# Kernel optimization log

Measured on AMD Instinct MI355X. Metric: run time of the kernel, lower is better.

Reference implementation:

```python
import jax, jax.numpy as jnp
import numpy as np

N_NODES = 100000
N_EDGES = 1600000
IN_F, HID, EMB = 128, 64, 32


def setup_inputs() -> dict:
    key = jax.random.key(0)
    ks = jax.random.split(key, 10)
    x = jax.random.normal(ks[0], (N_NODES, IN_F), dtype=jnp.float32)
    edge_index = jax.random.randint(ks[1], (2, N_EDGES), 0, N_NODES, dtype=jnp.int64)
    s = lambda k, sh, fan_in: jax.random.normal(k, sh, dtype=jnp.float32) / jnp.sqrt(jnp.float32(fan_in))
    return {
        "x": x,
        "edge_index": edge_index,
        # SAGEConv1: lin_l (applied to aggregated neighbors, with bias) + lin_r (root, no bias)
        "W1_l": s(ks[2], (IN_F, HID), IN_F), "b1": jnp.zeros((HID,), jnp.float32), "W1_r": s(ks[3], (IN_F, HID), IN_F),
        # SAGEConv2
        "W2_l": s(ks[4], (HID, EMB), HID), "b2": jnp.zeros((EMB,), jnp.float32), "W2_r": s(ks[5], (HID, EMB), HID),
        # risk head
        "Wh": s(ks[6], (EMB, 1), EMB), "bh": jnp.zeros((1,), jnp.float32),
    }


def _sage_conv(x, src, dst, W_l, b, W_r):
    # gather messages from source nodes, segment-mean at destination nodes
    msg_sum = jax.ops.segment_sum(x[src], dst, num_segments=N_NODES)  # [N, F]
    cnt = jax.ops.segment_sum(jnp.ones((src.shape[0],), x.dtype), dst, num_segments=N_NODES)
    mean_agg = msg_sum / jnp.maximum(cnt, 1.0)[:, None]  # isolated nodes -> 0
    return mean_agg @ W_l + b + x @ W_r


def reference(x, edge_index, W1_l, b1, W1_r, W2_l, b2, W2_r, Wh, bh):
    src, dst = edge_index[0], edge_index[1]
    h = jax.nn.relu(_sage_conv(x, src, dst, W1_l, b1, W1_r))
    # dropout is identity in eval mode
    embeddings = jax.nn.relu(_sage_conv(h, src, dst, W2_l, b2, W2_r))
    risk_scores = embeddings @ Wh + bh
    return embeddings, risk_scores
```

## Files before the change

### kernel.cpp

```cpp
#include <hip/hip_runtime.h>
#include <hip/hip_bf16.h>

#define N_NODES 100000
#define N_EDGES 1600000
#define NBUCK   196
#define BSHIFT  9
#define BCAP    12288

typedef __bf16 bf16x8 __attribute__((ext_vector_type(8)));
typedef float  f32x4  __attribute__((ext_vector_type(4)));
typedef float  f32x2  __attribute__((ext_vector_type(2)));


__device__ inline unsigned char enc_fp8(float v) {
    return (unsigned char)(__builtin_amdgcn_cvt_pk_fp8_f32(v, v, 0, 0) & 0xFF);
}

__global__ __launch_bounds__(256) void partition_k(const int* __restrict__ ei,
                                                   int* __restrict__ gcur,
                                                   unsigned* __restrict__ bbuf) {
    __shared__ int hist[NBUCK];
    __shared__ int cur[NBUCK];
    int t = threadIdx.x;
    for (int i = t; i < NBUCK; i += 256) hist[i] = 0;
    __syncthreads();
    int base = blockIdx.x * 4096;
    unsigned pk[16];
    int bk[16];
#pragma unroll
    for (int i = 0; i < 16; ++i) {
        int e = base + t + i * 256;
        if (e < N_EDGES) {
            int s = ei[e], d = ei[N_EDGES + e];
            int b = d >> BSHIFT;
            pk[i] = ((unsigned)(d & 511) << 17) | (unsigned)s;
            bk[i] = b;
            atomicAdd(&hist[b], 1);
        } else bk[i] = -1;
    }
    __syncthreads();
    for (int i = t; i < NBUCK; i += 256)
        cur[i] = atomicAdd(&gcur[i], hist[i]);
    __syncthreads();
#pragma unroll
    for (int i = 0; i < 16; ++i) {
        if (bk[i] >= 0) {
            int pos = atomicAdd(&cur[bk[i]], 1);
            bbuf[(size_t)bk[i] * BCAP + pos] = pk[i];
        }
    }
}

__global__ __launch_bounds__(256) void bucketcsr_k(const unsigned* __restrict__ bbuf,
                                                   const int* __restrict__ gcur,
                                                   int* __restrict__ cnt,
                                                   int* __restrict__ offsets,
                                                   int* __restrict__ csr) {
    __shared__ int lcnt[512];
    __shared__ int loff[512];
    __shared__ int lcur[512];
    __shared__ int ssum[256];
    int b = blockIdx.x, t = threadIdx.x;
    int m = gcur[b];
    const unsigned* src = bbuf + (size_t)b * BCAP;
    for (int i = t; i < 512; i += 256) lcnt[i] = 0;
    __syncthreads();
    for (int i = t; i < m; i += 256) atomicAdd(&lcnt[src[i] >> 17], 1);
    __syncthreads();
    int a0 = lcnt[2 * t], a1 = lcnt[2 * t + 1];
    int p0 = (a0 + 3) & ~3, p1 = (a1 + 3) & ~3;
    ssum[t] = p0 + p1;
    __syncthreads();
    for (int off = 1; off < 256; off <<= 1) {
        int v = (t >= off) ? ssum[t - off] : 0;
        __syncthreads();
        ssum[t] += v;
        __syncthreads();
    }
    int ebase = (t == 0) ? 0 : ssum[t - 1];
    loff[2 * t] = ebase;
    loff[2 * t + 1] = ebase + p0;
    __syncthreads();
    for (int i = t; i < 512; i += 256) lcur[i] = loff[i];
    int nbase = b << BSHIFT;
    for (int i = t; i < 512; i += 256) {
        int n = nbase + i;
        if (n < N_NODES) {
            cnt[n] = lcnt[i];
            offsets[n] = b * BCAP + loff[i];
        }
    }
    __syncthreads();
    for (int i = t; i < m; i += 256) {
        unsigned p = src[i];
        int pos = atomicAdd(&lcur[p >> 17], 1);
        csr[(size_t)b * BCAP + pos] = (int)(p & 0x1FFFF);
    }
}

__global__ __launch_bounds__(256) void gemm1_k(const float* __restrict__ x,
                                               const float* __restrict__ W1l,
                                               const float* __restrict__ W1r,
                                               unsigned char* __restrict__ c1l,
                                               __bf16* __restrict__ c1r) {
    __shared__ __bf16 Bt[128 * 136];
    int tid = threadIdx.x;
    for (int idx = tid; idx < 8192; idx += 256) {
        int k = idx >> 6, n = idx & 63;
        Bt[n * 136 + k]        = (__bf16)W1l[idx];
        Bt[(n + 64) * 136 + k] = (__bf16)W1r[idx];
    }
    __syncthreads();

    int lane = tid & 63, wave = tid >> 6;
    int mbase = blockIdx.x * 64 + wave * 16;
    int col  = lane & 15;
    int kgrp = (lane >> 4) << 3;
    int mrow = mbase + col;
    int mclamp = mrow < N_NODES ? mrow : N_NODES - 1;
    const float* arow = x + (size_t)mclamp * 128;

    f32x4 acc[8];
#pragma unroll
    for (int i = 0; i < 8; ++i) acc[i] = (f32x4){0.f, 0.f, 0.f, 0.f};

#pragma unroll
    for (int ks = 0; ks < 4; ++ks) {
        int kk = ks * 32 + kgrp;
        f32x4 a0 = *(const f32x4*)(arow + kk);
        f32x4 a1 = *(const f32x4*)(arow + kk + 4);
        bf16x8 a;
#pragma unroll
        for (int i = 0; i < 4; ++i) { a[i] = (__bf16)a0[i]; a[i + 4] = (__bf16)a1[i]; }
#pragma unroll
        for (int nt = 0; nt < 8; ++nt) {
            bf16x8 b = *(const bf16x8*)(Bt + (nt * 16 + col) * 136 + kk);
            acc[nt] = __builtin_amdgcn_mfma_f32_16x16x32_bf16(a, b, acc[nt], 0, 0, 0);
        }
    }

    int r0 = mbase + ((lane >> 4) << 2);
#pragma unroll
    for (int r = 0; r < 4; ++r) {
        int m = r0 + r;
        if (m < N_NODES) {
#pragma unroll
            for (int nt = 0; nt < 4; ++nt)
                c1l[(size_t)m * 64 + nt * 16 + col] = enc_fp8(acc[nt][r]);
#pragma unroll
            for (int nt = 4; nt < 8; ++nt)
                c1r[(size_t)m * 64 + (nt - 4) * 16 + col] = (__bf16)acc[nt][r];
        }
    }
}

__global__ __launch_bounds__(256) void agg1_k(const unsigned char* __restrict__ c1l,
                                              const __bf16* __restrict__ c1r,
                                              const int* __restrict__ offsets,
                                              const int* __restrict__ cnt,
                                              const int* __restrict__ csr,
                                              const float* __restrict__ b1,
                                              __bf16* __restrict__ h) {
    int wave = blockIdx.x * 4 + (threadIdx.x >> 6);
    int lane = threadIdx.x & 63;
    int g = lane >> 3;
    int n = wave * 8 + g;
    int f8b = (lane & 7) << 3;
    int beg = offsets[n], deg = cnt[n];
    int end = beg + deg;
    bf16x8 rv = *(const bf16x8*)(c1r + (size_t)n * 64 + f8b);
    const int4* csr4 = (const int4*)csr;
    float sum[8];
#pragma unroll
    for (int j = 0; j < 8; ++j) sum[j] = 0.f;
    for (int e = beg; e < end; e += 8) {
        int4 i0 = csr4[e >> 2];
        int4 i1 = csr4[(e >> 2) + 1];
        int sidx[8] = {i0.x, i0.y, i0.z, i0.w, i1.x, i1.y, i1.z, i1.w};
        uint2 w[8];
#pragma unroll
        for (int u = 0; u < 8; ++u) {
            w[u].x = 0u; w[u].y = 0u;
            if (e + u < end)
                w[u] = *(const uint2*)(c1l + (size_t)sidx[u] * 64 + f8b);
        }
#pragma unroll
        for (int u = 0; u < 8; ++u) {
            f32x2 p0 = __builtin_amdgcn_cvt_pk_f32_fp8(w[u].x, 0);
            f32x2 p1 = __builtin_amdgcn_cvt_pk_f32_fp8(w[u].x, 1);
            f32x2 p2 = __builtin_amdgcn_cvt_pk_f32_fp8(w[u].y, 0);
            f32x2 p3 = __builtin_amdgcn_cvt_pk_f32_fp8(w[u].y, 1);
            sum[0] += p0[0]; sum[1] += p0[1];
            sum[2] += p1[0]; sum[3] += p1[1];
            sum[4] += p2[0]; sum[5] += p2[1];
            sum[6] += p3[0]; sum[7] += p3[1];
        }
    }
    float cf = deg > 0 ? (float)deg : 1.f;
    bf16x8 o;
#pragma unroll
    for (int j = 0; j < 8; ++j) {
        float v = sum[j] / cf + (float)rv[j] + b1[f8b + j];
        o[j] = (__bf16)(v > 0.f ? v : 0.f);
    }
    *(bf16x8*)(h + (size_t)n * 64 + f8b) = o;
}

__global__ __launch_bounds__(256) void gemm2_k(const __bf16* __restrict__ h,
                                               const float* __restrict__ W2l,
                                               const float* __restrict__ W2r,
                                               unsigned char* __restrict__ c2l,
                                               float* __restrict__ c2r) {
    __shared__ __bf16 Bt[64 * 72];
    int tid = threadIdx.x;
    for (int idx = tid; idx < 2048; idx += 256) {
        int k = idx >> 5, n = idx & 31;
        Bt[n * 72 + k]        = (__bf16)W2l[idx];
        Bt[(n + 32) * 72 + k] = (__bf16)W2r[idx];
    }
    __syncthreads();

    int lane = tid & 63, wave = tid >> 6;
    int mbase = blockIdx.x * 64 + wave * 16;
    int col  = lane & 15;
    int kgrp = (lane >> 4) << 3;
    int mrow = mbase + col;
    int mclamp = mrow < N_NODES ? mrow : N_NODES - 1;
    const __bf16* arow = h + (size_t)mclamp * 64;

    f32x4 acc[4];
#pragma unroll
    for (int i = 0; i < 4; ++i) acc[i] = (f32x4){0.f, 0.f, 0.f, 0.f};

#pragma unroll
    for (int ks = 0; ks < 2; ++ks) {
        int kk = ks * 32 + kgrp;
        bf16x8 a = *(const bf16x8*)(arow + kk);
#pragma unroll
        for (int nt = 0; nt < 4; ++nt) {
            bf16x8 b = *(const bf16x8*)(Bt + (nt * 16 + col) * 72 + kk);
            acc[nt] = __builtin_amdgcn_mfma_f32_16x16x32_bf16(a, b, acc[nt], 0, 0, 0);
        }
    }

    int r0 = mbase + ((lane >> 4) << 2);
#pragma unroll
    for (int r = 0; r < 4; ++r) {
        int m = r0 + r;
        if (m < N_NODES) {
#pragma unroll
            for (int nt = 0; nt < 2; ++nt)
                c2l[(size_t)m * 32 + nt * 16 + col] = enc_fp8(acc[nt][r]);
#pragma unroll
            for (int nt = 2; nt < 4; ++nt)
                c2r[(size_t)m * 32 + (nt - 2) * 16 + col] = acc[nt][r];
        }
    }
}

__global__ __launch_bounds__(256) void agg2_k(const unsigned char* __restrict__ c2l,
                                              const float* __restrict__ c2r,
                                              const int* __restrict__ offsets,
                                              const int* __restrict__ cnt,
                                              const int* __restrict__ csr,
                                              const float* __restrict__ b2,
                                              const float* __restrict__ Wh,
                                              const float* __restrict__ bh,
                                              float* __restrict__ out) {
    int wave = blockIdx.x * 4 + (threadIdx.x >> 6);
    int lane = threadIdx.x & 63;
    int g = lane >> 2;
    int n = wave * 16 + g;
    int f8b = (lane & 3) << 3;
    bool valid = n < N_NODES;
    int nc = valid ? n : N_NODES - 1;
    int beg = offsets[nc], deg = valid ? cnt[n] : 0;
    int end = beg + deg;
    f32x4 rr0 = *(const f32x4*)(c2r + (size_t)nc * 32 + f8b);
    f32x4 rr1 = *(const f32x4*)(c2r + (size_t)nc * 32 + f8b + 4);
    f32x4 wh0 = *(const f32x4*)(Wh + f8b);
    f32x4 wh1 = *(const f32x4*)(Wh + f8b + 4);
    const int4* csr4 = (const int4*)csr;
    float sum[8];
#pragma unroll
    for (int j = 0; j < 8; ++j) sum[j] = 0.f;
    for (int e = beg; e < end; e += 8) {
        int4 i0 = csr4[e >> 2];
        int4 i1 = csr4[(e >> 2) + 1];
        int sidx[8] = {i0.x, i0.y, i0.z, i0.w, i1.x, i1.y, i1.z, i1.w};
        uint2 w[8];
#pragma unroll
        for (int u = 0; u < 8; ++u) {
            w[u].x = 0u; w[u].y = 0u;
            if (e + u < end)
                w[u] = *(const uint2*)(c2l + (size_t)sidx[u] * 32 + f8b);
        }
#pragma unroll
        for (int u = 0; u < 8; ++u) {
            f32x2 p0 = __builtin_amdgcn_cvt_pk_f32_fp8(w[u].x, 0);
            f32x2 p1 = __builtin_amdgcn_cvt_pk_f32_fp8(w[u].x, 1);
            f32x2 p2 = __builtin_amdgcn_cvt_pk_f32_fp8(w[u].y, 0);
            f32x2 p3 = __builtin_amdgcn_cvt_pk_f32_fp8(w[u].y, 1);
            sum[0] += p0[0]; sum[1] += p0[1];
            sum[2] += p1[0]; sum[3] += p1[1];
            sum[4] += p2[0]; sum[5] += p2[1];
            sum[6] += p3[0]; sum[7] += p3[1];
        }
    }
    float cf = deg > 0 ? (float)deg : 1.f;
    float r = 0.f;
    f32x4 o0, o1;
#pragma unroll
    for (int j = 0; j < 8; ++j) {
        float root = (j < 4) ? rr0[j] : rr1[j - 4];
        float whj  = (j < 4) ? wh0[j] : wh1[j - 4];
        float v = sum[j] / cf + root + b2[f8b + j];
        v = v > 0.f ? v : 0.f;
        if (j < 4) o0[j] = v; else o1[j - 4] = v;
        r += v * whj;
    }
    if (valid) {
        *(f32x4*)(out + (size_t)n * 32 + f8b) = o0;
        *(f32x4*)(out + (size_t)n * 32 + f8b + 4) = o1;
    }
    r += __shfl_xor(r, 1, 64);
    r += __shfl_xor(r, 2, 64);
    if (valid && (lane & 3) == 0)
        out[(size_t)N_NODES * 32 + n] = r + bh[0];
}

extern "C" void kernel_launch(void* const* d_in, const int* in_sizes, int n_in,
                              void* d_out, int out_size, void* d_ws, size_t ws_size,
                              hipStream_t stream) {
    const float* x   = (const float*)d_in[0];
    const int*   ei  = (const int*)d_in[1];
    const float* W1l = (const float*)d_in[2];
    const float* b1  = (const float*)d_in[3];
    const float* W1r = (const float*)d_in[4];
    const float* W2l = (const float*)d_in[5];
    const float* b2  = (const float*)d_in[6];
    const float* W2r = (const float*)d_in[7];
    const float* Wh  = (const float*)d_in[8];
    const float* bh  = (const float*)d_in[9];
    float* out = (float*)d_out;

    char* ws = (char*)d_ws;
    unsigned char* c1l = (unsigned char*)(ws);
    __bf16*   c1r     = (__bf16*)(ws + 6400000);
    __bf16*   h       = (__bf16*)(ws + 19200000);
    unsigned char* c2l = (unsigned char*)(ws + 32000000);
    float*    c2r     = (float*)(ws + 35200000);
    int*      cnt     = (int*)(ws + 48000000);
    int*      offsets = (int*)(ws + 48400000);
    int*      gcur    = (int*)(ws + 48800000);
    unsigned* bbuf    = (unsigned*)(ws + 48804096);
    int*      csr     = (int*)(ws + 58437888);

    hipMemsetAsync(gcur, 0, NBUCK * 4, stream);

    partition_k<<<391, 256, 0, stream>>>(ei, gcur, bbuf);
    bucketcsr_k<<<NBUCK, 256, 0, stream>>>(bbuf, gcur, cnt, offsets, csr);
    gemm1_k    <<<1563, 256, 0, stream>>>(x, W1l, W1r, c1l, c1r);
    agg1_k     <<<3125, 256, 0, stream>>>(c1l, c1r, offsets, cnt, csr, b1, h);
    gemm2_k    <<<1563, 256, 0, stream>>>(h, W2l, W2r, c2l, c2r);
    agg2_k     <<<1563, 256, 0, stream>>>(c2l, c2r, offsets, cnt, csr, b2, Wh, bh, out);
}
```

Before: 221.0 us.

## Merge CSR build with gemm1 and fuse layer-1 aggregation into gemm2

The bucket-to-CSR pass and the first GEMM are independent, so they now run as one launch: the first NBUCK blocks build the CSR and the remaining blocks do the x·W1 GEMM. The layer-1 mean aggregation is fused into the second GEMM, with each block aggregating 64 nodes into a shared-memory tile of h and running the MFMA on it directly. This removes two launches and the global write and re-read of h. In exchange the fused kernel holds more LDS per block, which may lower occupancy, and each wave now aggregates two node groups serially.

```diff
diff --git a/kernel.cpp b/kernel.cpp
--- a/kernel.cpp
+++ b/kernel.cpp
@@ -51,182 +51,190 @@
     }
 }
 
-__global__ __launch_bounds__(256) void bucketcsr_k(const unsigned* __restrict__ bbuf,
+__global__ __launch_bounds__(256) void csr_gemm1_k(const unsigned* __restrict__ bbuf,
                                                    const int* __restrict__ gcur,
                                                    int* __restrict__ cnt,
                                                    int* __restrict__ offsets,
-                                                   int* __restrict__ csr) {
-    __shared__ int lcnt[512];
-    __shared__ int loff[512];
-    __shared__ int lcur[512];
-    __shared__ int ssum[256];
-    int b = blockIdx.x, t = threadIdx.x;
-    int m = gcur[b];
-    const unsigned* src = bbuf + (size_t)b * BCAP;
-    for (int i = t; i < 512; i += 256) lcnt[i] = 0;
-    __syncthreads();
-    for (int i = t; i < m; i += 256) atomicAdd(&lcnt[src[i] >> 17], 1);
-    __syncthreads();
-    int a0 = lcnt[2 * t], a1 = lcnt[2 * t + 1];
-    int p0 = (a0 + 3) & ~3, p1 = (a1 + 3) & ~3;
-    ssum[t] = p0 + p1;
-    __syncthreads();
-    for (int off = 1; off < 256; off <<= 1) {
-        int v = (t >= off) ? ssum[t - off] : 0;
-        __syncthreads();
-        ssum[t] += v;
-        __syncthreads();
-    }
-    int ebase = (t == 0) ? 0 : ssum[t - 1];
-    loff[2 * t] = ebase;
-    loff[2 * t + 1] = ebase + p0;
-    __syncthreads();
-    for (int i = t; i < 512; i += 256) lcur[i] = loff[i];
-    int nbase = b << BSHIFT;
-    for (int i = t; i < 512; i += 256) {
-        int n = nbase + i;
-        if (n < N_NODES) {
-            cnt[n] = lcnt[i];
-            offsets[n] = b * BCAP + loff[i];
-        }
-    }
-    __syncthreads();
-    for (int i = t; i < m; i += 256) {
-        unsigned p = src[i];
-        int pos = atomicAdd(&lcur[p >> 17], 1);
-        csr[(size_t)b * BCAP + pos] = (int)(p & 0x1FFFF);
-    }
-}
-
-__global__ __launch_bounds__(256) void gemm1_k(const float* __restrict__ x,
-                                               const float* __restrict__ W1l,
-                                               const float* __restrict__ W1r,
-                                               unsigned char* __restrict__ c1l,
-                                               __bf16* __restrict__ c1r) {
-    __shared__ __bf16 Bt[128 * 136];
-    int tid = threadIdx.x;
-    for (int idx = tid; idx < 8192; idx += 256) {
-        int k = idx >> 6, n = idx & 63;
-        Bt[n * 136 + k]        = (__bf16)W1l[idx];
-        Bt[(n + 64) * 136 + k] = (__bf16)W1r[idx];
-    }
-    __syncthreads();
-
-    int lane = tid & 63, wave = tid >> 6;
-    int mbase = blockIdx.x * 64 + wave * 16;
-    int col  = lane & 15;
-    int kgrp = (lane >> 4) << 3;
-    int mrow = mbase + col;
-    int mclamp = mrow < N_NODES ? mrow : N_NODES - 1;
-    const float* arow = x + (size_t)mclamp * 128;
-
-    f32x4 acc[8];
-#pragma unroll
-    for (int i = 0; i < 8; ++i) acc[i] = (f32x4){0.f, 0.f, 0.f, 0.f};
-
-#pragma unroll
-    for (int ks = 0; ks < 4; ++ks) {
-        int kk = ks * 32 + kgrp;
-        f32x4 a0 = *(const f32x4*)(arow + kk);
-        f32x4 a1 = *(const f32x4*)(arow + kk + 4);
-        bf16x8 a;
-#pragma unroll
-        for (int i = 0; i < 4; ++i) { a[i] = (__bf16)a0[i]; a[i + 4] = (__bf16)a1[i]; }
-#pragma unroll
-        for (int nt = 0; nt < 8; ++nt) {
-            bf16x8 b = *(const bf16x8*)(Bt + (nt * 16 + col) * 136 + kk);
-            acc[nt] = __builtin_amdgcn_mfma_f32_16x16x32_bf16(a, b, acc[nt], 0, 0, 0);
-        }
-    }
-
-    int r0 = mbase + ((lane >> 4) << 2);
-#pragma unroll
-    for (int r = 0; r < 4; ++r) {
-        int m = r0 + r;
-        if (m < N_NODES) {
-#pragma unroll
-            for (int nt = 0; nt < 4; ++nt)
-                c1l[(size_t)m * 64 + nt * 16 + col] = enc_fp8(acc[nt][r]);
-#pragma unroll
-            for (int nt = 4; nt < 8; ++nt)
-                c1r[(size_t)m * 64 + (nt - 4) * 16 + col] = (__bf16)acc[nt][r];
-        }
-    }
-}
-
-__global__ __launch_bounds__(256) void agg1_k(const unsigned char* __restrict__ c1l,
-                                              const __bf16* __restrict__ c1r,
-                                              const int* __restrict__ offsets,
-                                              const int* __restrict__ cnt,
-                                              const int* __restrict__ csr,
-                                              const float* __restrict__ b1,
-                                              __bf16* __restrict__ h) {
-    int wave = blockIdx.x * 4 + (threadIdx.x >> 6);
-    int lane = threadIdx.x & 63;
-    int g = lane >> 3;
-    int n = wave * 8 + g;
-    int f8b = (lane & 7) << 3;
-    int beg = offsets[n], deg = cnt[n];
-    int end = beg + deg;
-    bf16x8 rv = *(const bf16x8*)(c1r + (size_t)n * 64 + f8b);
-    const int4* csr4 = (const int4*)csr;
-    float sum[8];
-#pragma unroll
-    for (int j = 0; j < 8; ++j) sum[j] = 0.f;
-    for (int e = beg; e < end; e += 8) {
-        int4 i0 = csr4[e >> 2];
-        int4 i1 = csr4[(e >> 2) + 1];
-        int sidx[8] = {i0.x, i0.y, i0.z, i0.w, i1.x, i1.y, i1.z, i1.w};
-        uint2 w[8];
-#pragma unroll
-        for (int u = 0; u < 8; ++u) {
-            w[u].x = 0u; w[u].y = 0u;
-            if (e + u < end)
-                w[u] = *(const uint2*)(c1l + (size_t)sidx[u] * 64 + f8b);
-        }
-#pragma unroll
-        for (int u = 0; u < 8; ++u) {
-            f32x2 p0 = __builtin_amdgcn_cvt_pk_f32_fp8(w[u].x, 0);
-            f32x2 p1 = __builtin_amdgcn_cvt_pk_f32_fp8(w[u].x, 1);
-            f32x2 p2 = __builtin_amdgcn_cvt_pk_f32_fp8(w[u].y, 0);
-            f32x2 p3 = __builtin_amdgcn_cvt_pk_f32_fp8(w[u].y, 1);
-            sum[0] += p0[0]; sum[1] += p0[1];
-            sum[2] += p1[0]; sum[3] += p1[1];
-            sum[4] += p2[0]; sum[5] += p2[1];
-            sum[6] += p3[0]; sum[7] += p3[1];
-        }
-    }
-    float cf = deg > 0 ? (float)deg : 1.f;
-    bf16x8 o;
-#pragma unroll
-    for (int j = 0; j < 8; ++j) {
-        float v = sum[j] / cf + (float)rv[j] + b1[f8b + j];
-        o[j] = (__bf16)(v > 0.f ? v : 0.f);
-    }
-    *(bf16x8*)(h + (size_t)n * 64 + f8b) = o;
-}
-
-__global__ __launch_bounds__(256) void gemm2_k(const __bf16* __restrict__ h,
-                                               const float* __restrict__ W2l,
-                                               const float* __restrict__ W2r,
-                                               unsigned char* __restrict__ c2l,
-                                               float* __restrict__ c2r) {
+                                                   int* __restrict__ csr,
+                                                   const float* __restrict__ x,
+                                                   const float* __restrict__ W1l,
+                                                   const float* __restrict__ W1r,
+                                                   unsigned char* __restrict__ c1l,
+                                                   __bf16* __restrict__ c1r) {
+    __shared__ __align__(16) char smem[34816];
+    int t = threadIdx.x;
+    if (blockIdx.x < NBUCK) {
+        int* lcnt = (int*)smem;
+        int* loff = (int*)(smem + 2048);
+        int* lcur = (int*)(smem + 4096);
+        int* ssum = (int*)(smem + 6144);
+        int b = blockIdx.x;
+        int m = gcur[b];
+        const unsigned* src = bbuf + (size_t)b * BCAP;
+        for (int i = t; i < 512; i += 256) lcnt[i] = 0;
+        __syncthreads();
+        for (int i = t; i < m; i += 256) atomicAdd(&lcnt[src[i] >> 17], 1);
+        __syncthreads();
+        int a0 = lcnt[2 * t], a1 = lcnt[2 * t + 1];
+        int p0 = (a0 + 3) & ~3, p1 = (a1 + 3) & ~3;
+        ssum[t] = p0 + p1;
+        __syncthreads();
+        for (int off = 1; off < 256; off <<= 1) {
+            int v = (t >= off) ? ssum[t - off] : 0;
+            __syncthreads();
+            ssum[t] += v;
+            __syncthreads();
+        }
+        int ebase = (t == 0) ? 0 : ssum[t - 1];
+        loff[2 * t] = ebase;
+        loff[2 * t + 1] = ebase + p0;
+        __syncthreads();
+        for (int i = t; i < 512; i += 256) lcur[i] = loff[i];
+        int nbase = b << BSHIFT;
+        for (int i = t; i < 512; i += 256) {
+            int n = nbase + i;
+            if (n < N_NODES) {
+                cnt[n] = lcnt[i];
+                offsets[n] = b * BCAP + loff[i];
+            }
+        }
+        __syncthreads();
+        for (int i = t; i < m; i += 256) {
+            unsigned p = src[i];
+            int pos = atomicAdd(&lcur[p >> 17], 1);
+            csr[(size_t)b * BCAP + pos] = (int)(p & 0x1FFFF);
+        }
+    } else {
+        __bf16* Bt = (__bf16*)smem;
+        for (int idx = t; idx < 8192; idx += 256) {
+            int k = idx >> 6, n = idx & 63;
+            Bt[n * 136 + k]        = (__bf16)W1l[idx];
+            Bt[(n + 64) * 136 + k] = (__bf16)W1r[idx];
+        }
+        __syncthreads();
+
+        int lane = t & 63, wave = t >> 6;
+        int bid = blockIdx.x - NBUCK;
+        int mbase = bid * 64 + wave * 16;
+        int col  = lane & 15;
+        int kgrp = (lane >> 4) << 3;
+        int mrow = mbase + col;
+        int mclamp = mrow < N_NODES ? mrow : N_NODES - 1;
+        const float* arow = x + (size_t)mclamp * 128;
+
+        f32x4 acc[8];
+#pragma unroll
+        for (int i = 0; i < 8; ++i) acc[i] = (f32x4){0.f, 0.f, 0.f, 0.f};
+
+#pragma unroll
+        for (int ks = 0; ks < 4; ++ks) {
+            int kk = ks * 32 + kgrp;
+            f32x4 a0 = *(const f32x4*)(arow + kk);
+            f32x4 a1 = *(const f32x4*)(arow + kk + 4);
+            bf16x8 a;
+#pragma unroll
+            for (int i = 0; i < 4; ++i) { a[i] = (__bf16)a0[i]; a[i + 4] = (__bf16)a1[i]; }
+#pragma unroll
+            for (int nt = 0; nt < 8; ++nt) {
+                bf16x8 b = *(const bf16x8*)(Bt + (nt * 16 + col) * 136 + kk);
+                acc[nt] = __builtin_amdgcn_mfma_f32_16x16x32_bf16(a, b, acc[nt], 0, 0, 0);
+            }
+        }
+
+        int r0 = mbase + ((lane >> 4) << 2);
+#pragma unroll
+        for (int r = 0; r < 4; ++r) {
+            int m = r0 + r;
+            if (m < N_NODES) {
+#pragma unroll
+                for (int nt = 0; nt < 4; ++nt)
+                    c1l[(size_t)m * 64 + nt * 16 + col] = enc_fp8(acc[nt][r]);
+#pragma unroll
+                for (int nt = 4; nt < 8; ++nt)
+                    c1r[(size_t)m * 64 + (nt - 4) * 16 + col] = (__bf16)acc[nt][r];
+            }
+        }
+    }
+}
+
+__global__ __launch_bounds__(256) void agg1_gemm2_k(const unsigned char* __restrict__ c1l,
+                                                    const __bf16* __restrict__ c1r,
+                                                    const int* __restrict__ offsets,
+                                                    const int* __restrict__ cnt,
+                                                    const int* __restrict__ csr,
+                                                    const float* __restrict__ b1,
+                                                    const float* __restrict__ W2l,
+                                                    const float* __restrict__ W2r,
+                                                    unsigned char* __restrict__ c2l,
+                                                    float* __restrict__ c2r) {
     __shared__ __bf16 Bt[64 * 72];
+    __shared__ __bf16 ht[64 * 72];
     int tid = threadIdx.x;
     for (int idx = tid; idx < 2048; idx += 256) {
         int k = idx >> 5, n = idx & 31;
         Bt[n * 72 + k]        = (__bf16)W2l[idx];
         Bt[(n + 32) * 72 + k] = (__bf16)W2r[idx];
     }
+
+    int lane = tid & 63, wave = tid >> 6;
+    int g = lane >> 3;
+    int f8b = (lane & 7) << 3;
+    f32x4 b1v0 = *(const f32x4*)(b1 + f8b);
+    f32x4 b1v1 = *(const f32x4*)(b1 + f8b + 4);
+    const int4* csr4 = (const int4*)csr;
+#pragma unroll
+    for (int p = 0; p < 2; ++p) {
+        int lrow = p * 32 + wave * 8 + g;
+        int n = blockIdx.x * 64 + lrow;
+        bf16x8 o;
+        if (n < N_NODES) {
+            int beg = offsets[n], deg = cnt[n];
+            int end = beg + deg;
+            bf16x8 rv = *(const bf16x8*)(c1r + (size_t)n * 64 + f8b);
+            float sum[8];
+#pragma unroll
+            for (int j = 0; j < 8; ++j) sum[j] = 0.f;
+            for (int e = beg; e < end; e += 8) {
+                int4 i0 = csr4[e >> 2];
+                int4 i1 = csr4[(e >> 2) + 1];
+                int sidx[8] = {i0.x, i0.y, i0.z, i0.w, i1.x, i1.y, i1.z, i1.w};
+                uint2 w[8];
+#pragma unroll
+                for (int u = 0; u < 8; ++u) {
+                    w[u].x = 0u; w[u].y = 0u;
+                    if (e + u < end)
+                        w[u] = *(const uint2*)(c1l + (size_t)sidx[u] * 64 + f8b);
+                }
+#pragma unroll
+                for (int u = 0; u < 8; ++u) {
+                    f32x2 p0 = __builtin_amdgcn_cvt_pk_f32_fp8(w[u].x, 0);
+                    f32x2 p1 = __builtin_amdgcn_cvt_pk_f32_fp8(w[u].x, 1);
+                    f32x2 p2 = __builtin_amdgcn_cvt_pk_f32_fp8(w[u].y, 0);
+                    f32x2 p3 = __builtin_amdgcn_cvt_pk_f32_fp8(w[u].y, 1);
+                    sum[0] += p0[0]; sum[1] += p0[1];
+                    sum[2] += p1[0]; sum[3] += p1[1];
+                    sum[4] += p2[0]; sum[5] += p2[1];
+                    sum[6] += p3[0]; sum[7] += p3[1];
+                }
+            }
+            float cf = deg > 0 ? (float)deg : 1.f;
+#pragma unroll
+            for (int j = 0; j < 8; ++j) {
+                float v = sum[j] / cf + (float)rv[j] + ((j < 4) ? b1v0[j] : b1v1[j - 4]);
+                o[j] = (__bf16)(v > 0.f ? v : 0.f);
+            }
+        } else {
+#pragma unroll
+            for (int j = 0; j < 8; ++j) o[j] = (__bf16)0.f;
+        }
+        *(bf16x8*)(ht + lrow * 72 + f8b) = o;
+    }
     __syncthreads();
 
-    int lane = tid & 63, wave = tid >> 6;
-    int mbase = blockIdx.x * 64 + wave * 16;
     int col  = lane & 15;
     int kgrp = (lane >> 4) << 3;
-    int mrow = mbase + col;
-    int mclamp = mrow < N_NODES ? mrow : N_NODES - 1;
-    const __bf16* arow = h + (size_t)mclamp * 64;
+    int mbase = blockIdx.x * 64 + wave * 16;
+    const __bf16* arow = ht + (wave * 16 + col) * 72;
 
     f32x4 acc[4];
 #pragma unroll
@@ -347,7 +355,6 @@
     char* ws = (char*)d_ws;
     unsigned char* c1l = (unsigned char*)(ws);
     __bf16*   c1r     = (__bf16*)(ws + 6400000);
-    __bf16*   h       = (__bf16*)(ws + 19200000);
     unsigned char* c2l = (unsigned char*)(ws + 32000000);
     float*    c2r     = (float*)(ws + 35200000);
     int*      cnt     = (int*)(ws + 48000000);
@@ -358,10 +365,10 @@
 
     hipMemsetAsync(gcur, 0, NBUCK * 4, stream);
 
-    partition_k<<<391, 256, 0, stream>>>(ei, gcur, bbuf);
-    bucketcsr_k<<<NBUCK, 256, 0, stream>>>(bbuf, gcur, cnt, offsets, csr);
-    gemm1_k    <<<1563, 256, 0, stream>>>(x, W1l, W1r, c1l, c1r);
-    agg1_k     <<<3125, 256, 0, stream>>>(c1l, c1r, offsets, cnt, csr, b1, h);
-    gemm2_k    <<<1563, 256, 0, stream>>>(h, W2l, W2r, c2l, c2r);
-    agg2_k     <<<1563, 256, 0, stream>>>(c2l, c2r, offsets, cnt, csr, b2, Wh, bh, out);
-}
+    partition_k  <<<391, 256, 0, stream>>>(ei, gcur, bbuf);
+    csr_gemm1_k  <<<NBUCK + 1563, 256, 0, stream>>>(bbuf, gcur, cnt, offsets, csr,
+                                                    x, W1l, W1r, c1l, c1r);
+    agg1_gemm2_k <<<1563, 256, 0, stream>>>(c1l, c1r, offsets, cnt, csr, b1,
+                                            W2l, W2r, c2l, c2r);
+    agg2_k       <<<1563, 256, 0, stream>>>(c2l, c2r, offsets, cnt, csr, b2, Wh, bh, out);
+}
```

Measured after the change: 212.0 us. -4.1%, faster.
